# Kernel tuning notes

Measured on AMD Instinct MI355X. Metric: run time of the kernel, lower is better.

Reference implementation:

```python
import jax, jax.numpy as jnp
import numpy as np

NUM_HEADS = 8  # config.num_heads


def setup_inputs() -> dict:
    key = jax.random.key(0)
    k0, k1, k2, k3, k4 = jax.random.split(key, 5)
    B, N, C, E = 32, 20000, 8, 512
    query_embeddings = jax.random.normal(k0, (B, E), dtype=jnp.float32)
    all_embeddings = jax.random.normal(k1, (N, E), dtype=jnp.float32)
    label_mask = jax.random.bernoulli(k2, 0.5, (N, C))  # bool multi-label mask
    # per-class MultiheadAttention q/k in-projection params (torch Linear convention: x @ W.T + b)
    Wq = jax.random.normal(k3, (C, E, E), dtype=jnp.float32) * 0.02
    Wk = jax.random.normal(k4, (C, E, E), dtype=jnp.float32) * 0.02
    bq = jnp.zeros((C, E), dtype=jnp.float32)
    bk = jnp.zeros((C, E), dtype=jnp.float32)
    return {
        "query_embeddings": query_embeddings,
        "all_embeddings": all_embeddings,
        "label_mask": label_mask,
        "Wq": Wq,
        "bq": bq,
        "Wk": Wk,
        "bk": bk,
        "n_samples": 5,
    }


def reference(query_embeddings, all_embeddings, label_mask, Wq, bq, Wk, bk, n_samples):
    """Vectorized-over-classes version of EmbeddingSelector.get_similar_samples.

    For each class c: q = query @ Wq[c].T + bq[c]; k_c over the class's database
    members; per-head scaled-dot softmax; attn weights averaged over heads
    (torch MHA need_weights default); top-k over class members. Non-members are
    masked to -inf before softmax, so they get weight 0 and (since every class
    has >> n_samples members) never enter the top-k -- identical math to the
    per-class gather loop, with global indices returned directly.
    """
    C, E, _ = Wq.shape
    H = NUM_HEADS
    dh = E // H
    B = query_embeddings.shape[0]
    N = all_embeddings.shape[0]

    # per-class projections (torch Linear: x @ W.T + b)
    q = jnp.einsum('be,cfe->cbf', query_embeddings, Wq) + bq[:, None, :]   # (C,B,E)
    k = jnp.einsum('ne,cfe->cnf', all_embeddings, Wk) + bk[:, None, :]     # (C,N,E)
    q = q.reshape(C, B, H, dh)
    k = k.reshape(C, N, H, dh)

    scale = 1.0 / jnp.sqrt(jnp.asarray(dh, q.dtype))
    scores = jnp.einsum('cbhd,cnhd->cbhn', q, k) * scale                   # (C,B,H,N)
    member = jnp.transpose(label_mask)[:, None, None, :]                   # (C,1,1,N)
    scores = jnp.where(member, scores, jnp.asarray(-1e9, scores.dtype))
    attn = jax.nn.softmax(scores, axis=-1).mean(axis=2)                    # (C,B,N) head-avg

    weights, indices = jax.lax.top_k(attn, n_samples)                      # (C,B,ns)
    result_weights = jnp.transpose(weights, (1, 0, 2))                     # (B,C,ns)
    result_indices = jnp.transpose(indices, (1, 0, 2)).astype(jnp.int32)   # (B,C,ns) global ids
    return result_indices, result_weights
```

## Files before the change

### kernel.cpp

```cpp
#include <hip/hip_runtime.h>
#include <math.h>

#define B_  32
#define N_  20000
#define C_  8
#define E_  512
#define H_  8
#define SCALE 0.125f
#define UNSC  9.765625e-4f

#define CHUNK 1024
#define NCH   20
#define NC3   157
#define NCG   20
#define SSZ ((size_t)B_ * H_ * N_)

typedef __attribute__((ext_vector_type(8))) _Float16 h8_t;
typedef __attribute__((ext_vector_type(8))) short   s8_t;
typedef __attribute__((ext_vector_type(4))) float f32x4;

#define MFMAH(a, b, c) __builtin_amdgcn_mfma_f32_16x16x32_f16(a, b, c, 0, 0, 0)

#define GLOAD_LDS16(g, l)                                              \
    __builtin_amdgcn_global_load_lds(                                  \
        (const __attribute__((address_space(1))) unsigned int*)(g),    \
        (__attribute__((address_space(3))) unsigned int*)(l), 16, 0, 0)

__device__ inline unsigned short f16_round(float x, float& fv) {
    _Float16 h = (_Float16)x;
    fv = (float)h;
    union { _Float16 hh; unsigned short us; } u;
    u.hh = h;
    return u.us;
}

__global__ __launch_bounds__(256) void k_q2(
        const float* __restrict__ x, const float* __restrict__ Wq,
        const float* __restrict__ bq, float* __restrict__ q) {
    int ft = blockIdx.x, c = blockIdx.y;
    int f0 = ft * 8;
    __shared__ float wsm[8][66];
    __shared__ float xs[32][66];
    int tid = threadIdx.x;
    int b = tid & 31, fs = tid >> 5;
    float acc = 0.f;
    const float* W = Wq + (size_t)c * E_ * E_;
    for (int k0 = 0; k0 < E_; k0 += 64) {
        __syncthreads();
        for (int i = tid; i < 512; i += 256)
            wsm[i >> 6][i & 63] = W[(size_t)(f0 + (i >> 6)) * E_ + k0 + (i & 63)];
        for (int i = tid; i < 2048; i += 256)
            xs[i >> 6][i & 63] = x[(size_t)(i >> 6) * E_ + k0 + (i & 63)];
        __syncthreads();
        #pragma unroll
        for (int kk = 0; kk < 64; ++kk)
            acc += xs[b][kk] * wsm[fs][kk];
    }
    q[((size_t)c * B_ + b) * E_ + f0 + fs] = acc + bq[c * E_ + f0 + fs];
}

__global__ __launch_bounds__(256) void k_u2(
        const float* __restrict__ q, const float* __restrict__ Wk,
        const float* __restrict__ bk, float* __restrict__ u,
        float* __restrict__ qb) {
    int et = blockIdx.x, h = blockIdx.y, c = blockIdx.z;
    int e0 = et * 64;
    __shared__ float qs[32][66];
    __shared__ float wk[64][66];
    int tid = threadIdx.x;
    int b = tid & 31, es = tid >> 5;
    for (int i = tid; i < 2048; i += 256)
        qs[i >> 6][i & 63] = q[((size_t)c * B_ + (i >> 6)) * E_ + h * 64 + (i & 63)];
    const float* W = Wk + (size_t)c * E_ * E_ + (size_t)(h * 64) * E_;
    for (int i = tid; i < 4096; i += 256)
        wk[i >> 6][i & 63] = W[(size_t)(i >> 6) * E_ + e0 + (i & 63)];
    __syncthreads();
    float acc[8] = {};
    for (int d = 0; d < 64; ++d) {
        float qv = qs[b][d];
        #pragma unroll
        for (int j = 0; j < 8; ++j)
            acc[j] += qv * wk[d][es * 8 + j];
    }
    float* urow = u + ((size_t)c * 256 + b * 8 + h) * E_ + e0 + es * 8;
    #pragma unroll
    for (int j = 0; j < 8; ++j) urow[j] = acc[j];
    if (et == 0 && es == 0) {
        float s = 0.f;
        const float* bkr = bk + c * E_ + h * 64;
        for (int d = 0; d < 64; ++d) s += qs[b][d] * bkr[d];
        qb[c * 256 + b * 8 + h] = s;
    }
}

#define U2P ((size_t)C_ * 16 * 16 * 512)

__global__ void k_split_u2(const float* __restrict__ u, short* __restrict__ u2) {
    int bx = blockIdx.x;
    int ks = bx & 15, mt = (bx >> 4) & 15, c = bx >> 8;
    int lane = threadIdx.x;
    int m  = mt * 16 + (lane & 15);
    int k0 = ks * 32 + (lane >> 4) * 8;
    const float* up = u + ((size_t)c * 256 + m) * 512 + k0;
    size_t base = ((((size_t)c * 16 + mt) * 16 + ks) * 512) + (size_t)lane * 8;
    s8_t vh, vm;
    #pragma unroll
    for (int j = 0; j < 8; ++j) {
        float x = up[j] * 32.0f, fh, fm;
        vh[j] = (short)f16_round(x, fh);
        vm[j] = (short)f16_round(x - fh, fm);
    }
    *(s8_t*)(u2 + base)       = vh;
    *(s8_t*)(u2 + U2P + base) = vm;
}

__global__ void k_split_A2(const float* __restrict__ A, short* __restrict__ A2t) {
    int nc = blockIdx.x, ks = blockIdx.y;
    int tid = threadIdx.x;
    int n = tid >> 1, kg = (tid & 1) * 2;
    int gn = nc * 128 + n;
    const float* ap = A + (size_t)gn * 512 + ks * 32 + kg * 8;
    s8_t vh[2], vm[2];
    #pragma unroll
    for (int g = 0; g < 2; ++g)
        #pragma unroll
        for (int j = 0; j < 8; ++j) {
            float x = (gn < N_) ? ap[g * 8 + j] * 32.0f : 0.f;
            float fh, fm;
            vh[g][j] = (short)f16_round(x, fh);
            vm[g][j] = (short)f16_round(x - fh, fm);
        }
    short* outp = A2t + ((size_t)nc * 16 + ks) * 8192 + n * 32;
    #pragma unroll
    for (int g = 0; g < 2; ++g) {
        int p = ((kg + g) + (n >> 1)) & 3;
        *(s8_t*)(outp + p * 8)        = vh[g];
        *(s8_t*)(outp + 4096 + p * 8) = vm[g];
    }
}

__global__ __launch_bounds__(256, 3) void k_scores_mfma(
        const short* __restrict__ u2, const short* __restrict__ A2t,
        const float* __restrict__ qb, const int* __restrict__ mask,
        float* __restrict__ S, float* __restrict__ Zpart, int c0, int CB) {
    __shared__ __align__(16) short As[16384];
    __shared__ float sQb[128];
    __shared__ int   sMask[128];
    int bx = blockIdx.x;
    int x     = bx & 7;
    int rest  = bx >> 3;
    int mh    = rest & 1;
    int rest2 = rest >> 1;
    int z     = rest2 % CB;
    int g     = rest2 / CB;
    int nc    = g * 8 + x;
    if (nc >= NC3) return;
    int c  = c0 + z;
    int tid = threadIdx.x;
    int lane = tid & 63, w = tid >> 6;
    int quad = lane >> 4, l15 = lane & 15;
    int n0 = nc * 128;

    if (tid < 128) {
        sQb[tid] = qb[c * 256 + mh * 128 + tid];
        int n = n0 + tid;
        sMask[tid] = (n < N_) ? mask[(size_t)n * C_ + c] : 0;
    }

    f32x4 acc[2][8];
    #pragma unroll
    for (int i = 0; i < 2; ++i)
        #pragma unroll
        for (int j = 0; j < 8; ++j)
            acc[i][j] = (f32x4){0.f, 0.f, 0.f, 0.f};

    const char* tb = (const char*)A2t + (size_t)nc * 262144;

    for (int ks2 = 0; ks2 < 8; ++ks2) {
        __syncthreads();
        const char* src = tb + (size_t)ks2 * 32768;
        #pragma unroll
        for (int t = 0; t < 8; ++t) {
            int seg = w * 8 + t;
            GLOAD_LDS16(src + (size_t)seg * 1024 + lane * 16,
                        (char*)As + seg * 1024);
        }
        __syncthreads();

        #pragma unroll
        for (int kh = 0; kh < 2; ++kh) {
            int ks = ks2 * 2 + kh;
            const short* Ab = As + kh * 8192;
            h8_t af[2][2];
            #pragma unroll
            for (int mt = 0; mt < 2; ++mt) {
                int mtg = mh * 8 + w * 2 + mt;
                size_t ub = ((((size_t)c * 16 + mtg) * 16 + ks) * 512)
                            + (size_t)lane * 8;
                af[mt][0] = *(const h8_t*)(u2 + ub);
                af[mt][1] = *(const h8_t*)(u2 + U2P + ub);
            }
            #pragma unroll
            for (int half = 0; half < 2; ++half) {
                __builtin_amdgcn_sched_barrier(0);
                #pragma unroll
                for (int q4 = 0; q4 < 4; ++q4) {
                    int nt = half * 4 + q4;
                    int r = nt * 16 + l15;
                    const short* bp = Ab + r * 32 + ((quad + (r >> 1)) & 3) * 8;
                    h8_t b0 = *(const h8_t*)bp;
                    h8_t b1 = *(const h8_t*)(bp + 4096);
                    #pragma unroll
                    for (int mt = 0; mt < 2; ++mt) {
                        f32x4 a = acc[mt][nt];
                        a = MFMAH(af[mt][0], b0, a);
                        a = MFMAH(af[mt][0], b1, a);
                        a = MFMAH(af[mt][1], b0, a);
                        acc[mt][nt] = a;
                    }
                }
            }
        }
    }

    float* Sc = S + (size_t)z * SSZ;
    #pragma unroll
    for (int mt = 0; mt < 2; ++mt) {
        float rs[4] = {0.f, 0.f, 0.f, 0.f};
        #pragma unroll
        for (int nt = 0; nt < 8; ++nt) {
            int nl = nt * 16 + l15;
            int n = n0 + nl;
            int mem = sMask[nl];
            #pragma unroll
            for (int r = 0; r < 4; ++r) {
                int ml = w * 32 + mt * 16 + quad * 4 + r;
                float sc = SCALE * (acc[mt][nt][r] * UNSC + sQb[ml]);
                float ev = mem ? __expf(sc) : 0.f;
                rs[r] += ev;
                if (n < N_) Sc[(size_t)(mh * 128 + ml) * N_ + n] = ev;
            }
        }
        #pragma unroll
        for (int r = 0; r < 4; ++r) {
            float v = rs[r];
            v += __shfl_xor(v, 1); v += __shfl_xor(v, 2);
            v += __shfl_xor(v, 4); v += __shfl_xor(v, 8);
            if (l15 == 0) {
                int ml = w * 32 + mt * 16 + quad * 4 + r;
                Zpart[((size_t)nc * C_ + c) * 256 + mh * 128 + ml] = v;
            }
        }
    }
}

__global__ void k_zsum(const float* __restrict__ Zpart, float* __restrict__ Z, int c0) {
    int c = c0 + blockIdx.x;
    int i = c * 256 + threadIdx.x;
    float s = 0.f;
    for (int nc = 0; nc < NC3; ++nc) s += Zpart[(size_t)nc * (C_ * 256) + i];
    Z[i] = s;
}

__global__ __launch_bounds__(256) void k_topk1(
        const float* __restrict__ S, const float* __restrict__ Z,
        float2* __restrict__ cand, int c0, int ns) {
    int chunk = blockIdx.x, b = blockIdx.y, z = blockIdx.z;
    const float* Sc = S + (size_t)z * SSZ;
    int tid = threadIdx.x;
    __shared__ float zr[H_];
    if (tid < H_) zr[tid] = 1.0f / Z[(c0 + z) * (B_ * H_) + b * H_ + tid];
    __syncthreads();
    int n0 = chunk * CHUNK + tid * 4;
    bool valid = n0 < N_;
    float4 a = make_float4(0.f, 0.f, 0.f, 0.f);
    if (valid) {
        #pragma unroll
        for (int h = 0; h < H_; ++h) {
            const float4 sv = *(const float4*)&Sc[(size_t)(b * H_ + h) * N_ + n0];
            float wz = zr[h];
            a.x += sv.x * wz; a.y += sv.y * wz; a.z += sv.z * wz; a.w += sv.w * wz;
        }
    }
    float v[4]; int ix[4];
    v[0] = valid ? a.x * 0.125f : -1.f;
    v[1] = valid ? a.y * 0.125f : -1.f;
    v[2] = valid ? a.z * 0.125f : -1.f;
    v[3] = valid ? a.w * 0.125f : -1.f;
    #pragma unroll
    for (int t = 0; t < 4; ++t) ix[t] = valid ? n0 + t : N_;

    __shared__ float wv[4];
    __shared__ int   wi[4];
    __shared__ int   winS;
    int lane = tid & 63, w = tid >> 6;
    for (int j = 0; j < ns; ++j) {
        float bv = v[0]; int bi = ix[0];
        #pragma unroll
        for (int t = 1; t < 4; ++t)
            if (v[t] > bv || (v[t] == bv && ix[t] < bi)) { bv = v[t]; bi = ix[t]; }
        #pragma unroll
        for (int off = 1; off < 64; off <<= 1) {
            float ov = __shfl_xor(bv, off, 64);
            int   oi = __shfl_xor(bi, off, 64);
            if (ov > bv || (ov == bv && oi < bi)) { bv = ov; bi = oi; }
        }
        if (lane == 0) { wv[w] = bv; wi[w] = bi; }
        __syncthreads();
        if (tid == 0) {
            float fv = wv[0]; int fi = wi[0];
            #pragma unroll
            for (int t = 1; t < 4; ++t)
                if (wv[t] > fv || (wv[t] == fv && wi[t] < fi)) { fv = wv[t]; fi = wi[t]; }
            cand[(((size_t)z * B_ + b) * NCH + chunk) * ns + j] =
                make_float2(fv, (float)fi);
            winS = fi;
        }
        __syncthreads();
        int wn = winS;
        #pragma unroll
        for (int t = 0; t < 4; ++t)
            if (ix[t] == wn) v[t] = -2.f;
    }
}

__global__ __launch_bounds__(256) void k_topk2(
        const float2* __restrict__ cand, float* __restrict__ out, int c0, int ns) {
    int b = blockIdx.x, z = blockIdx.y;
    int c = c0 + z;
    int tid = threadIdx.x;
    int ncand = NCH * ns;
    const float2* cb = cand + ((size_t)z * B_ + b) * ncand;
    float v = -3.f; int ix = N_ + 1;
    if (tid < ncand) { float2 e = cb[tid]; v = e.x; ix = (int)e.y; }
    __shared__ float sv[256];
    __shared__ int   si[256];
    __shared__ int   win;
    for (int j = 0; j < ns; ++j) {
        sv[tid] = v; si[tid] = ix;
        __syncthreads();
        for (int w = 128; w >= 1; w >>= 1) {
            if (tid < w) {
                float v2 = sv[tid + w]; int i2 = si[tid + w];
                if (v2 > sv[tid] || (v2 == sv[tid] && i2 < si[tid])) {
                    sv[tid] = v2; si[tid] = i2;
                }
            }
            __syncthreads();
        }
        if (tid == 0) {
            out[((size_t)b * C_ + c) * ns + j] = (float)si[0];
            out[(size_t)B_ * C_ * ns + ((size_t)b * C_ + c) * ns + j] = sv[0];
            win = si[0];
        }
        __syncthreads();
        if (ix == win) v = -3.f;
        __syncthreads();
    }
}

extern "C" void kernel_launch(void* const* d_in, const int* in_sizes, int n_in,
                              void* d_out, int out_size, void* d_ws, size_t ws_size,
                              hipStream_t stream) {
    const float* x    = (const float*)d_in[0];
    const float* A    = (const float*)d_in[1];
    const int*   mask = (const int*)  d_in[2];
    const float* Wq   = (const float*)d_in[3];
    const float* bq   = (const float*)d_in[4];
    const float* Wk   = (const float*)d_in[5];
    const float* bk   = (const float*)d_in[6];
    float* out = (float*)d_out;

    int ns = out_size / (2 * B_ * C_);

    float* ws = (float*)d_ws;
    float* q     = ws;
    float* u     = q     + (size_t)C_ * B_ * E_;
    float* qb    = u     + (size_t)C_ * B_ * H_ * E_;
    float* Z     = qb    + (size_t)C_ * B_ * H_;
    float* Zpart = Z     + (size_t)C_ * B_ * H_;
    short* u2    = (short*)(Zpart + (size_t)NC3 * C_ * 256);
    short* A2t   = u2 + 2 * U2P;
    float* S     = (float*)(A2t + (size_t)NC3 * 16 * 8192);
    size_t fixedFloats = (size_t)(S - ws);

    size_t candFloats = (size_t)C_ * B_ * NCH * ns * 2;
    int CB = 8;
    while (CB > 1 &&
           (fixedFloats + (size_t)CB * SSZ + candFloats + 16) * 4 > ws_size)
        CB >>= 1;
    float2* cand = (float2*)(S + (size_t)CB * SSZ);

    k_q2<<<dim3(64, C_), 256, 0, stream>>>(x, Wq, bq, q);
    k_u2<<<dim3(8, H_, C_), 256, 0, stream>>>(q, Wk, bk, u, qb);
    k_split_u2<<<C_ * 16 * 16, 64, 0, stream>>>(u, u2);
    k_split_A2<<<dim3(NC3, 16), 256, 0, stream>>>(A, A2t);

    for (int c0 = 0; c0 < C_; c0 += CB) {
        k_scores_mfma<<<NCG * 2 * 8 * CB, 256, 0, stream>>>(u2, A2t, qb, mask, S, Zpart, c0, CB);
        k_zsum<<<CB, 256, 0, stream>>>(Zpart, Z, c0);
        k_topk1<<<dim3(NCH, B_, CB), 256, 0, stream>>>(S, Z, cand, c0, ns);
        k_topk2<<<dim3(B_, CB), 256, 0, stream>>>(cand, out, c0, ns);
    }
}
```

Before: 373.3 us.

## Fuse u2 fp16 split into k_u2, raise score occupancy, per-warp top-k merge

Folds the fp16 hi/lo split of u into the k_u2 epilogue, which drops the separate k_split_u2 kernel and the fp32 u buffer round trip. It also raises the launch-bounds occupancy hint for the MFMA scores kernel from 3 to 4 blocks per CU. The top-k chunk kernel now has each warp take its own top ns candidates without block barriers per step, and one thread merges the 4*ns warp candidates at the end. The per-warp selection keeps the same candidates, but the 32-bit used mask limits ns to 8, and a dead leftover loop remains in the merge.

New measurement: 394.3 us. 5.6% more time.

```diff
diff --git a/kernel.cpp b/kernel.cpp
--- a/kernel.cpp
+++ b/kernel.cpp
@@ -59,9 +59,11 @@
     q[((size_t)c * B_ + b) * E_ + f0 + fs] = acc + bq[c * E_ + f0 + fs];
 }
 
+#define U2P ((size_t)C_ * 16 * 16 * 512)
+
 __global__ __launch_bounds__(256) void k_u2(
         const float* __restrict__ q, const float* __restrict__ Wk,
-        const float* __restrict__ bk, float* __restrict__ u,
+        const float* __restrict__ bk, short* __restrict__ u2,
         float* __restrict__ qb) {
     int et = blockIdx.x, h = blockIdx.y, c = blockIdx.z;
     int e0 = et * 64;
@@ -82,9 +84,21 @@
         for (int j = 0; j < 8; ++j)
             acc[j] += qv * wk[d][es * 8 + j];
     }
-    float* urow = u + ((size_t)c * 256 + b * 8 + h) * E_ + e0 + es * 8;
-    #pragma unroll
-    for (int j = 0; j < 8; ++j) urow[j] = acc[j];
+    int m   = b * 8 + h;
+    int e0s = e0 + es * 8;
+    int ks  = e0s >> 5, quad = (e0s & 31) >> 3;
+    int lane = (m & 15) + 16 * quad;
+    int mt  = m >> 4;
+    size_t base = ((((size_t)c * 16 + mt) * 16 + ks) * 512) + (size_t)lane * 8;
+    s8_t vh, vm;
+    #pragma unroll
+    for (int j = 0; j < 8; ++j) {
+        float xv = acc[j] * 32.0f, fh, fm;
+        vh[j] = (short)f16_round(xv, fh);
+        vm[j] = (short)f16_round(xv - fh, fm);
+    }
+    *(s8_t*)(u2 + base)       = vh;
+    *(s8_t*)(u2 + U2P + base) = vm;
     if (et == 0 && es == 0) {
         float s = 0.f;
         const float* bkr = bk + c * E_ + h * 64;
@@ -93,27 +107,6 @@
     }
 }
 
-#define U2P ((size_t)C_ * 16 * 16 * 512)
-
-__global__ void k_split_u2(const float* __restrict__ u, short* __restrict__ u2) {
-    int bx = blockIdx.x;
-    int ks = bx & 15, mt = (bx >> 4) & 15, c = bx >> 8;
-    int lane = threadIdx.x;
-    int m  = mt * 16 + (lane & 15);
-    int k0 = ks * 32 + (lane >> 4) * 8;
-    const float* up = u + ((size_t)c * 256 + m) * 512 + k0;
-    size_t base = ((((size_t)c * 16 + mt) * 16 + ks) * 512) + (size_t)lane * 8;
-    s8_t vh, vm;
-    #pragma unroll
-    for (int j = 0; j < 8; ++j) {
-        float x = up[j] * 32.0f, fh, fm;
-        vh[j] = (short)f16_round(x, fh);
-        vm[j] = (short)f16_round(x - fh, fm);
-    }
-    *(s8_t*)(u2 + base)       = vh;
-    *(s8_t*)(u2 + U2P + base) = vm;
-}
-
 __global__ void k_split_A2(const float* __restrict__ A, short* __restrict__ A2t) {
     int nc = blockIdx.x, ks = blockIdx.y;
     int tid = threadIdx.x;
@@ -139,7 +132,7 @@
     }
 }
 
-__global__ __launch_bounds__(256, 3) void k_scores_mfma(
+__global__ __launch_bounds__(256, 4) void k_scores_mfma(
         const short* __restrict__ u2, const short* __restrict__ A2t,
         const float* __restrict__ qb, const int* __restrict__ mask,
         float* __restrict__ S, float* __restrict__ Zpart, int c0, int CB) {
@@ -290,9 +283,8 @@
     #pragma unroll
     for (int t = 0; t < 4; ++t) ix[t] = valid ? n0 + t : N_;
 
-    __shared__ float wv[4];
-    __shared__ int   wi[4];
-    __shared__ int   winS;
+    __shared__ float wv[4][8];
+    __shared__ int   wi[4][8];
     int lane = tid & 63, w = tid >> 6;
     for (int j = 0; j < ns; ++j) {
         float bv = v[0]; int bi = ix[0];
@@ -305,22 +297,34 @@
             int   oi = __shfl_xor(bi, off, 64);
             if (ov > bv || (ov == bv && oi < bi)) { bv = ov; bi = oi; }
         }
-        if (lane == 0) { wv[w] = bv; wi[w] = bi; }
-        __syncthreads();
-        if (tid == 0) {
-            float fv = wv[0]; int fi = wi[0];
-            #pragma unroll
-            for (int t = 1; t < 4; ++t)
-                if (wv[t] > fv || (wv[t] == fv && wi[t] < fi)) { fv = wv[t]; fi = wi[t]; }
-            cand[(((size_t)z * B_ + b) * NCH + chunk) * ns + j] =
-                make_float2(fv, (float)fi);
-            winS = fi;
-        }
-        __syncthreads();
-        int wn = winS;
+        if (lane == 0) { wv[w][j] = bv; wi[w][j] = bi; }
         #pragma unroll
         for (int t = 0; t < 4; ++t)
-            if (ix[t] == wn) v[t] = -2.f;
+            if (ix[t] == bi) v[t] = -2.f;
+    }
+    __syncthreads();
+    if (tid == 0) {
+        unsigned used = 0;
+        float2* cp = cand + (((size_t)z * B_ + b) * NCH + chunk) * ns;
+        for (int j = 0; j < ns; ++j) {
+            float fv = -4.f; int fi = N_ + 1; int fs = -1;
+            for (int s2 = 0; s2 < 4 * ns; ++s2) {
+                if (used & (1u << s2)) continue;
+                float cv = wv[s2 >> 3][s2 & 7];
+                int   ci = wi[s2 >> 3][s2 & 7];
+                (void)cv; (void)ci;
+                break;
+            }
+            for (int w2 = 0; w2 < 4; ++w2)
+                for (int t = 0; t < ns; ++t) {
+                    int s2 = w2 * ns + t;
+                    if (used & (1u << s2)) continue;
+                    float cv = wv[w2][t]; int ci = wi[w2][t];
+                    if (cv > fv || (cv == fv && ci < fi)) { fv = cv; fi = ci; fs = s2; }
+                }
+            used |= (1u << fs);
+            cp[j] = make_float2(fv, (float)fi);
+        }
     }
 }
 
@@ -375,8 +379,7 @@
 
     float* ws = (float*)d_ws;
     float* q     = ws;
-    float* u     = q     + (size_t)C_ * B_ * E_;
-    float* qb    = u     + (size_t)C_ * B_ * H_ * E_;
+    float* qb    = q     + (size_t)C_ * B_ * E_;
     float* Z     = qb    + (size_t)C_ * B_ * H_;
     float* Zpart = Z     + (size_t)C_ * B_ * H_;
     short* u2    = (short*)(Zpart + (size_t)NC3 * C_ * 256);
@@ -392,8 +395,7 @@
     float2* cand = (float2*)(S + (size_t)CB * SSZ);
 
     k_q2<<<dim3(64, C_), 256, 0, stream>>>(x, Wq, bq, q);
-    k_u2<<<dim3(8, H_, C_), 256, 0, stream>>>(q, Wk, bk, u, qb);
-    k_split_u2<<<C_ * 16 * 16, 64, 0, stream>>>(u, u2);
+    k_u2<<<dim3(8, H_, C_), 256, 0, stream>>>(q, Wk, bk, u2, qb);
     k_split_A2<<<dim3(NC3, 16), 256, 0, stream>>>(A, A2t);
 
     for (int c0 = 0; c0 < C_; c0 += CB) {
```
